# Performance work log

Hardware: AMD Instinct MI355X
Metric: run time of the kernel (lower is better)

Reference implementation:

```python
import jax, jax.numpy as jnp
import numpy as np

N_NODES = 50000


def _gcn_conv(x, edge_index, W, b, n_nodes):
    # PyG GCNConv: add self loops, symmetric normalization, then
    # out[dst] = sum_{src->dst} norm * (x[src] @ W) + b
    src, dst = edge_index[0], edge_index[1]
    loop = jnp.arange(n_nodes, dtype=src.dtype)
    src = jnp.concatenate([src, loop])
    dst = jnp.concatenate([dst, loop])
    deg = jax.ops.segment_sum(jnp.ones_like(src, dtype=x.dtype), dst, num_segments=n_nodes)
    dinv = jnp.where(deg > 0, jax.lax.rsqrt(deg), 0.0)
    norm = dinv[src] * dinv[dst]                      # [E+N]
    h = x @ W                                         # [N, out] dense GEMM first (in >= out here)
    msg = h[src] * norm[:, None]                      # gather + scale
    out = jax.ops.segment_sum(msg, dst, num_segments=n_nodes)  # scatter-add
    return out + b


def setup_inputs() -> dict:
    key = jax.random.key(0)
    k = jax.random.split(key, 5)
    in_c, hid_c, out_c = 128, 128, 64
    n, e = N_NODES, 800000
    x = jax.random.normal(k[0], (n, in_c), dtype=jnp.float32)
    edge_index = jax.random.randint(k[1], (2, e), 0, n, dtype=jnp.int64)
    # Glorot-ish scaled weights
    W1 = jax.random.normal(k[2], (in_c, hid_c), dtype=jnp.float32) * (1.0 / np.sqrt(in_c))
    b1 = jnp.zeros((hid_c,), dtype=jnp.float32)
    W2 = jax.random.normal(k[3], (hid_c, out_c), dtype=jnp.float32) * (1.0 / np.sqrt(hid_c))
    b2 = jnp.zeros((out_c,), dtype=jnp.float32)
    return {"x": x, "edge_index": edge_index, "W1": W1, "b1": b1, "W2": W2, "b2": b2}


def reference(x, edge_index, W1, b1, W2, b2):
    # Net.encode: conv1 -> relu -> conv2
    h = _gcn_conv(x, edge_index, W1, b1, N_NODES)
    h = jax.nn.relu(h)
    z = _gcn_conv(h, edge_index, W2, b2, N_NODES)
    return z
```

## Files before the change

### kernel.cpp

```cpp
#include <hip/hip_runtime.h>
#include <math.h>

constexpr int C_IN  = 128;
constexpr int C_HID = 128;
constexpr int C_OUT = 64;
constexpr int NREP  = 8;

typedef short bf8   __attribute__((ext_vector_type(8)));
typedef float f32x4 __attribute__((ext_vector_type(4)));

__device__ __forceinline__ int wave_incl_scan(int v, int lane) {
    #pragma unroll
    for (int off = 1; off < 64; off <<= 1) {
        int u = __shfl_up(v, off, 64);
        if (lane >= off) v += u;
    }
    return v;
}
__device__ __forceinline__ short b16(float f) {
    unsigned int u = __float_as_uint(f);
    u += 0x7FFFu + ((u >> 16) & 1u);
    return (short)(u >> 16);
}
__device__ __forceinline__ unsigned int bpack(float a, float b) {
    unsigned int ua = __float_as_uint(a), ub = __float_as_uint(b);
    ua += 0x7FFFu + ((ua >> 16) & 1u);
    ub += 0x7FFFu + ((ub >> 16) & 1u);
    return (ua >> 16) | (ub & 0xFFFF0000u);
}
__device__ __forceinline__ void acc4(float* a, const uint2 v) {
    a[0] += __uint_as_float(v.x << 16);
    a[1] += __uint_as_float(v.x & 0xFFFF0000u);
    a[2] += __uint_as_float(v.y << 16);
    a[3] += __uint_as_float(v.y & 0xFFFF0000u);
}
__device__ __forceinline__ void acc8(float* a, const uint4 v) {
    a[0] += __uint_as_float(v.x << 16);
    a[1] += __uint_as_float(v.x & 0xFFFF0000u);
    a[2] += __uint_as_float(v.y << 16);
    a[3] += __uint_as_float(v.y & 0xFFFF0000u);
    a[4] += __uint_as_float(v.z << 16);
    a[5] += __uint_as_float(v.z & 0xFFFF0000u);
    a[6] += __uint_as_float(v.w << 16);
    a[7] += __uint_as_float(v.w & 0xFFFF0000u);
}

__global__ __launch_bounds__(256) void k_zero(int* __restrict__ p, int n4) {
    int i = blockIdx.x * 256 + threadIdx.x;
    if (i < n4) reinterpret_cast<int4*>(p)[i] = make_int4(0, 0, 0, 0);
}

__global__ __launch_bounds__(256) void k_count2r(const int* __restrict__ dst, int e, int n,
                                                 int* __restrict__ cntr,
                                                 int* __restrict__ slot) {
    int i = blockIdx.x * 256 + threadIdx.x;
    if (i >= e) return;
    int r = blockIdx.x & (NREP - 1);
    slot[i] = atomicAdd(&cntr[r * n + dst[i]], 1);
}

__global__ __launch_bounds__(256) void k_scanA8(int* __restrict__ cntr, int n,
                                                int* __restrict__ rowstart,
                                                int* __restrict__ blocksum,
                                                float* __restrict__ dinv) {
    __shared__ int swave[4];
    const int tid = threadIdx.x, lane = tid & 63, w = tid >> 6;
    const int idx = blockIdx.x * 1024 + tid * 4;
    int4 c = make_int4(0, 0, 0, 0);
    if (idx + 3 < n) {
        #pragma unroll
        for (int r = 0; r < NREP; ++r) {
            int4* p = reinterpret_cast<int4*>(cntr + (size_t)r * n + idx);
            int4 t = *p;
            *p = c;
            c.x += t.x; c.y += t.y; c.z += t.z; c.w += t.w;
        }
    } else if (idx < n) {
        for (int m = idx; m < n; ++m) {
            int acc = 0;
            #pragma unroll
            for (int r = 0; r < NREP; ++r) {
                int t = cntr[(size_t)r * n + m];
                cntr[(size_t)r * n + m] = acc;
                acc += t;
            }
            int q = m - idx;
            if (q == 0) c.x = acc; else if (q == 1) c.y = acc;
            else if (q == 2) c.z = acc; else c.w = acc;
        }
    }
    if (idx + 0 < n) dinv[idx + 0] = rsqrtf((float)(c.x + 1));
    if (idx + 1 < n) dinv[idx + 1] = rsqrtf((float)(c.y + 1));
    if (idx + 2 < n) dinv[idx + 2] = rsqrtf((float)(c.z + 1));
    if (idx + 3 < n) dinv[idx + 3] = rsqrtf((float)(c.w + 1));

    const int s4 = c.x + c.y + c.z + c.w;
    const int incl = wave_incl_scan(s4, lane);
    if (lane == 63) swave[w] = incl;
    __syncthreads();
    int base = incl - s4;
    #pragma unroll
    for (int j = 0; j < 4; ++j) if (j < w) base += swave[j];

    int4 o;
    o.x = base;
    o.y = base + c.x;
    o.z = base + c.x + c.y;
    o.w = base + c.x + c.y + c.z;
    if (idx < n) *reinterpret_cast<int4*>(rowstart + idx) = o;

    if (tid == 0) blocksum[blockIdx.x] = swave[0] + swave[1] + swave[2] + swave[3];
}

__global__ __launch_bounds__(64) void k_scanB(const int* __restrict__ blocksum, int nb,
                                              int* __restrict__ blockoff,
                                              int* __restrict__ rowstart, int n) {
    const int lane = threadIdx.x;
    int v = (lane < nb) ? blocksum[lane] : 0;
    int incl = wave_incl_scan(v, lane);
    if (lane < nb) blockoff[lane] = incl - v;
    if (lane == 63) rowstart[n] = incl;
}

__global__ __launch_bounds__(256) void k_scanC(int* __restrict__ rowstart,
                                               const int* __restrict__ blockoff, int n) {
    const int idx = (blockIdx.x * 256 + threadIdx.x) * 4;
    if (idx >= n) return;
    const int off = blockoff[idx >> 10];
    if (idx + 3 < n) {
        int4 v = *reinterpret_cast<int4*>(rowstart + idx);
        v.x += off; v.y += off; v.z += off; v.w += off;
        *reinterpret_cast<int4*>(rowstart + idx) = v;
    } else {
        for (int i = idx; i < n; ++i) rowstart[i] += off;
    }
}

__global__ __launch_bounds__(256) void k_fill2r(const int* __restrict__ src,
                                                const int* __restrict__ dst,
                                                const int* __restrict__ slot, int e, int n,
                                                const int* __restrict__ rowstart,
                                                const int* __restrict__ repoff,
                                                unsigned short* __restrict__ nbr) {
    int i = blockIdx.x * 256 + threadIdx.x;
    if (i >= e) return;
    int r = blockIdx.x & (NREP - 1);
    int d = dst[i];
    int pos = rowstart[d] + repoff[r * n + d] + slot[i];
    nbr[pos] = (unsigned short)src[i];
}

__global__ __launch_bounds__(256) void k_gemm1m(const float* __restrict__ x,
                                                const float* __restrict__ W,
                                                const float* __restrict__ dinv,
                                                unsigned short* __restrict__ h1b,
                                                int n) {
    __shared__ short wf[8 * 4 * 64 * 8];
    const int tid = threadIdx.x;

    for (int i = tid; i < 2048; i += 256) {
        const int l = i & 63, kt = (i >> 6) & 3, ct = i >> 8;
        const int krow = kt * 32 + ((l >> 4) << 3);
        const int col  = ct * 16 + (l & 15);
        const float* wp = W + (size_t)krow * C_HID + col;
        uint4 u;
        u.x = bpack(wp[0 * C_HID], wp[1 * C_HID]);
        u.y = bpack(wp[2 * C_HID], wp[3 * C_HID]);
        u.z = bpack(wp[4 * C_HID], wp[5 * C_HID]);
        u.w = bpack(wp[6 * C_HID], wp[7 * C_HID]);
        reinterpret_cast<uint4*>(wf)[i] = u;
    }
    __syncthreads();

    const int l = tid & 63, w = tid >> 6;
    const int row0 = blockIdx.x * 64 + w * 16;
    int arow = row0 + (l & 15);
    if (arow >= n) arow = n - 1;
    const float* xr = x + (size_t)arow * C_IN + ((l >> 4) << 3);

    bf8 a[4];
    #pragma unroll
    for (int kt = 0; kt < 4; ++kt) {
        float4 p0 = *reinterpret_cast<const float4*>(xr + kt * 32);
        float4 p1 = *reinterpret_cast<const float4*>(xr + kt * 32 + 4);
        bf8 t;
        t[0] = b16(p0.x); t[1] = b16(p0.y); t[2] = b16(p0.z); t[3] = b16(p0.w);
        t[4] = b16(p1.x); t[5] = b16(p1.y); t[6] = b16(p1.z); t[7] = b16(p1.w);
        a[kt] = t;
    }

    f32x4 acc[8];
    #pragma unroll
    for (int ct = 0; ct < 8; ++ct) acc[ct] = (f32x4){0.f, 0.f, 0.f, 0.f};
    const bf8* bw = reinterpret_cast<const bf8*>(wf);
    #pragma unroll
    for (int kt = 0; kt < 4; ++kt)
        #pragma unroll
        for (int ct = 0; ct < 8; ++ct)
            acc[ct] = __builtin_amdgcn_mfma_f32_16x16x32_bf16(
                a[kt], bw[(ct * 4 + kt) * 64 + l], acc[ct], 0, 0, 0);

    const int rbase = row0 + ((l >> 4) << 2);
    float dv[4];
    #pragma unroll
    for (int r = 0; r < 4; ++r) {
        int rr = rbase + r;
        dv[r] = (rr < n) ? dinv[rr] : 0.f;
    }
    #pragma unroll
    for (int ct = 0; ct < 8; ++ct) {
        const int col = ct * 16 + (l & 15);
        #pragma unroll
        for (int r = 0; r < 4; ++r) {
            int rr = rbase + r;
            if (rr < n)
                h1b[(size_t)rr * C_HID + col] = (unsigned short)b16(acc[ct][r] * dv[r]);
        }
    }
}

__global__ __launch_bounds__(256) void k_agg1b(const unsigned int* __restrict__ h1b,
                                               const int* __restrict__ rowstart,
                                               const unsigned short* __restrict__ nbr,
                                               const float* __restrict__ dinv,
                                               const float* __restrict__ b1,
                                               unsigned int* __restrict__ actb,
                                               int n) {
    int node = blockIdx.x * 8 + (threadIdx.x >> 5);
    if (node >= n) return;
    const int c4 = threadIdx.x & 31;
    const uint2* h1v = reinterpret_cast<const uint2*>(h1b);
    float a[4] = {0.f, 0.f, 0.f, 0.f};
    acc4(a, h1v[node * 32 + c4]);
    int j   = rowstart[node];
    int end = rowstart[node + 1];
    for (; j + 1 < end; j += 2) {
        int s0 = nbr[j], s1 = nbr[j + 1];
        uint2 v0 = h1v[s0 * 32 + c4];
        uint2 v1 = h1v[s1 * 32 + c4];
        acc4(a, v0); acc4(a, v1);
    }
    if (j < end) acc4(a, h1v[nbr[j] * 32 + c4]);
    const float sc = dinv[node];
    const float4 bb = reinterpret_cast<const float4*>(b1)[c4];
    uint2 p;
    p.x = bpack(fmaxf(sc * a[0] + bb.x, 0.f), fmaxf(sc * a[1] + bb.y, 0.f));
    p.y = bpack(fmaxf(sc * a[2] + bb.z, 0.f), fmaxf(sc * a[3] + bb.w, 0.f));
    reinterpret_cast<uint2*>(actb)[node * 32 + c4] = p;
}

__global__ __launch_bounds__(256) void k_gemm2m(const unsigned short* __restrict__ actb,
                                                const float* __restrict__ W2,
                                                const float* __restrict__ dinv,
                                                unsigned short* __restrict__ h2b,
                                                int n) {
    __shared__ short wf[4 * 4 * 64 * 8];
    const int tid = threadIdx.x;

    for (int i = tid; i < 1024; i += 256) {
        const int l = i & 63, kt = (i >> 6) & 3, ct = i >> 8;
        const int krow = kt * 32 + ((l >> 4) << 3);
        const int col  = ct * 16 + (l & 15);
        const float* wp = W2 + (size_t)krow * C_OUT + col;
        uint4 u;
        u.x = bpack(wp[0 * C_OUT], wp[1 * C_OUT]);
        u.y = bpack(wp[2 * C_OUT], wp[3 * C_OUT]);
        u.z = bpack(wp[4 * C_OUT], wp[5 * C_OUT]);
        u.w = bpack(wp[6 * C_OUT], wp[7 * C_OUT]);
        reinterpret_cast<uint4*>(wf)[i] = u;
    }
    __syncthreads();

    const int l = tid & 63, w = tid >> 6;
    const int row0 = blockIdx.x * 64 + w * 16;
    int arow = row0 + (l & 15);
    if (arow >= n) arow = n - 1;
    const unsigned short* ar = actb + (size_t)arow * C_HID + ((l >> 4) << 3);

    bf8 a[4];
    #pragma unroll
    for (int kt = 0; kt < 4; ++kt)
        a[kt] = *reinterpret_cast<const bf8*>(ar + kt * 32);

    f32x4 acc[4];
    #pragma unroll
    for (int ct = 0; ct < 4; ++ct) acc[ct] = (f32x4){0.f, 0.f, 0.f, 0.f};
    const bf8* bw = reinterpret_cast<const bf8*>(wf);
    #pragma unroll
    for (int kt = 0; kt < 4; ++kt)
        #pragma unroll
        for (int ct = 0; ct < 4; ++ct)
            acc[ct] = __builtin_amdgcn_mfma_f32_16x16x32_bf16(
                a[kt], bw[(ct * 4 + kt) * 64 + l], acc[ct], 0, 0, 0);

    const int rbase = row0 + ((l >> 4) << 2);
    float dv[4];
    #pragma unroll
    for (int r = 0; r < 4; ++r) {
        int rr = rbase + r;
        dv[r] = (rr < n) ? dinv[rr] : 0.f;
    }
    #pragma unroll
    for (int ct = 0; ct < 4; ++ct) {
        const int col = ct * 16 + (l & 15);
        #pragma unroll
        for (int r = 0; r < 4; ++r) {
            int rr = rbase + r;
            if (rr < n)
                h2b[(size_t)rr * C_OUT + col] = (unsigned short)b16(acc[ct][r] * dv[r]);
        }
    }
}

__global__ __launch_bounds__(256) void k_agg2b(const unsigned int* __restrict__ h2b,
                                               const int* __restrict__ rowstart,
                                               const unsigned short* __restrict__ nbr,
                                               const float* __restrict__ dinv,
                                               const float* __restrict__ b2,
                                               float* __restrict__ outb, int n) {
    int node = blockIdx.x * 32 + (threadIdx.x >> 3);
    if (node >= n) return;
    const int lane8 = threadIdx.x & 7;
    const uint4* h2v = reinterpret_cast<const uint4*>(h2b);
    float a8[8] = {0.f, 0.f, 0.f, 0.f, 0.f, 0.f, 0.f, 0.f};
    acc8(a8, h2v[node * 8 + lane8]);
    int j   = rowstart[node];
    int end = rowstart[node + 1];
    for (; j + 1 < end; j += 2) {
        int s0 = nbr[j], s1 = nbr[j + 1];
        uint4 v0 = h2v[s0 * 8 + lane8];
        uint4 v1 = h2v[s1 * 8 + lane8];
        acc8(a8, v0); acc8(a8, v1);
    }
    if (j < end) acc8(a8, h2v[nbr[j] * 8 + lane8]);
    const float s = dinv[node];
    const float4 c0 = reinterpret_cast<const float4*>(b2)[2 * lane8 + 0];
    const float4 c1 = reinterpret_cast<const float4*>(b2)[2 * lane8 + 1];
    float4 o0, o1;
    o0.x = s * a8[0] + c0.x; o0.y = s * a8[1] + c0.y;
    o0.z = s * a8[2] + c0.z; o0.w = s * a8[3] + c0.w;
    o1.x = s * a8[4] + c1.x; o1.y = s * a8[5] + c1.y;
    o1.z = s * a8[6] + c1.z; o1.w = s * a8[7] + c1.w;
    reinterpret_cast<float4*>(outb)[node * 16 + 2 * lane8 + 0] = o0;
    reinterpret_cast<float4*>(outb)[node * 16 + 2 * lane8 + 1] = o1;
}

extern "C" void kernel_launch(void* const* d_in, const int* in_sizes, int n_in,
                              void* d_out, int out_size, void* d_ws, size_t ws_size,
                              hipStream_t stream) {
    const float* x  = (const float*)d_in[0];
    const int*   ei = (const int*)d_in[1];
    const float* W1 = (const float*)d_in[2];
    const float* b1 = (const float*)d_in[3];
    const float* W2 = (const float*)d_in[4];
    const float* b2 = (const float*)d_in[5];

    const int n = in_sizes[0] / C_IN;
    const int e = in_sizes[1] / 2;
    const int* src = ei;
    const int* dst = ei + e;

    char* ws = (char*)d_ws;
    float* dinv     = (float*)(ws);
    int*   rowstart = (int*)  (ws + (2u << 18));
    int*   blocksum = (int*)  (ws + (1u << 20));
    int*   blockoff = (int*)  (ws + (1u << 20) + 4096);
    int*   cntr     = (int*)  (ws + (2u << 20));
    int*   slot     = (int*)  (ws + (4u << 20));
    unsigned short* nbr  = (unsigned short*)(ws + (8u << 20));
    unsigned short* h1b  = (unsigned short*)(ws + (10u << 20));
    unsigned short* actb = (unsigned short*)(ws + (23u << 20));
    unsigned short* h2b  = (unsigned short*)(ws + (36u << 20));
    float* outb     = (float*)d_out;

    const int NB = (n + 1023) / 1024;
    const int nz4 = (NREP * n + 3) / 4;

    k_zero   <<<(nz4 + 255) / 256, 256, 0, stream>>>(cntr, nz4);
    k_count2r<<<(e + 255) / 256, 256, 0, stream>>>(dst, e, n, cntr, slot);
    k_scanA8 <<<NB, 256, 0, stream>>>(cntr, n, rowstart, blocksum, dinv);
    k_scanB  <<<1, 64, 0, stream>>>(blocksum, NB, blockoff, rowstart, n);
    k_scanC  <<<NB, 256, 0, stream>>>(rowstart, blockoff, n);
    k_fill2r <<<(e + 255) / 256, 256, 0, stream>>>(src, dst, slot, e, n, rowstart, cntr, nbr);
    k_gemm1m <<<(n + 63) / 64, 256, 0, stream>>>(x, W1, dinv, h1b, n);
    k_agg1b  <<<(n + 7) / 8,   256, 0, stream>>>((const unsigned int*)h1b, rowstart, nbr, dinv, b1,
                                                 (unsigned int*)actb, n);
    k_gemm2m <<<(n + 63) / 64, 256, 0, stream>>>(actb, W2, dinv, h2b, n);
    k_agg2b  <<<(n + 31) / 32, 256, 0, stream>>>((const unsigned int*)h2b, rowstart, nbr, dinv, b2,
                                                 outb, n);
}
```

Baseline: 139.7 us.

## Merge scan kernels via last-block ticket, vectorize CSR build and widen agg1 loads

The three scan kernels become one, and the cross-block offset scan is done by the last block to finish, found with an atomic ticket. Consumers now add blockoff on the fly instead of running a separate fix-up pass. The edge count and fill kernels each handle four edges per thread with int4 loads. The layer-1 aggregation uses 16 lanes with 16-byte loads per node instead of 32 lanes with 8-byte loads. This removes two launches and the extra rowstart pass, at the cost of extra blockoff lookups in the gather and aggregation kernels and reliance on threadfence ordering.

```diff
diff --git a/kernel.cpp b/kernel.cpp
--- a/kernel.cpp
+++ b/kernel.cpp
@@ -27,12 +27,6 @@
     ua += 0x7FFFu + ((ua >> 16) & 1u);
     ub += 0x7FFFu + ((ub >> 16) & 1u);
     return (ua >> 16) | (ub & 0xFFFF0000u);
-}
-__device__ __forceinline__ void acc4(float* a, const uint2 v) {
-    a[0] += __uint_as_float(v.x << 16);
-    a[1] += __uint_as_float(v.x & 0xFFFF0000u);
-    a[2] += __uint_as_float(v.y << 16);
-    a[3] += __uint_as_float(v.y & 0xFFFF0000u);
 }
 __device__ __forceinline__ void acc8(float* a, const uint4 v) {
     a[0] += __uint_as_float(v.x << 16);
@@ -50,20 +44,35 @@
     if (i < n4) reinterpret_cast<int4*>(p)[i] = make_int4(0, 0, 0, 0);
 }
 
-__global__ __launch_bounds__(256) void k_count2r(const int* __restrict__ dst, int e, int n,
-                                                 int* __restrict__ cntr,
-                                                 int* __restrict__ slot) {
+__global__ __launch_bounds__(256) void k_count2r4(const int* __restrict__ dst, int e, int n,
+                                                  int* __restrict__ cntr,
+                                                  int* __restrict__ slot) {
     int i = blockIdx.x * 256 + threadIdx.x;
-    if (i >= e) return;
+    int base = i * 4;
+    if (base >= e) return;
     int r = blockIdx.x & (NREP - 1);
-    slot[i] = atomicAdd(&cntr[r * n + dst[i]], 1);
-}
-
-__global__ __launch_bounds__(256) void k_scanA8(int* __restrict__ cntr, int n,
-                                                int* __restrict__ rowstart,
-                                                int* __restrict__ blocksum,
-                                                float* __restrict__ dinv) {
+    int* c = cntr + (size_t)r * n;
+    if (base + 3 < e) {
+        int4 d4 = *reinterpret_cast<const int4*>(dst + base);
+        int4 s4;
+        s4.x = atomicAdd(&c[d4.x], 1);
+        s4.y = atomicAdd(&c[d4.y], 1);
+        s4.z = atomicAdd(&c[d4.z], 1);
+        s4.w = atomicAdd(&c[d4.w], 1);
+        *reinterpret_cast<int4*>(slot + base) = s4;
+    } else {
+        for (int q = base; q < e; ++q) slot[q] = atomicAdd(&c[dst[q]], 1);
+    }
+}
+
+__global__ __launch_bounds__(256) void k_scanAB8(int* __restrict__ cntr, int n,
+                                                 int* __restrict__ rowstart,
+                                                 int* __restrict__ blocksum,
+                                                 int* __restrict__ blockoff,
+                                                 int* __restrict__ ticket,
+                                                 float* __restrict__ dinv) {
     __shared__ int swave[4];
+    __shared__ int amLast;
     const int tid = threadIdx.x, lane = tid & 63, w = tid >> 6;
     const int idx = blockIdx.x * 1024 + tid * 4;
     int4 c = make_int4(0, 0, 0, 0);
@@ -102,52 +111,64 @@
     #pragma unroll
     for (int j = 0; j < 4; ++j) if (j < w) base += swave[j];
 
-    int4 o;
-    o.x = base;
-    o.y = base + c.x;
-    o.z = base + c.x + c.y;
-    o.w = base + c.x + c.y + c.z;
-    if (idx < n) *reinterpret_cast<int4*>(rowstart + idx) = o;
-
-    if (tid == 0) blocksum[blockIdx.x] = swave[0] + swave[1] + swave[2] + swave[3];
-}
-
-__global__ __launch_bounds__(64) void k_scanB(const int* __restrict__ blocksum, int nb,
-                                              int* __restrict__ blockoff,
-                                              int* __restrict__ rowstart, int n) {
-    const int lane = threadIdx.x;
-    int v = (lane < nb) ? blocksum[lane] : 0;
-    int incl = wave_incl_scan(v, lane);
-    if (lane < nb) blockoff[lane] = incl - v;
-    if (lane == 63) rowstart[n] = incl;
-}
-
-__global__ __launch_bounds__(256) void k_scanC(int* __restrict__ rowstart,
-                                               const int* __restrict__ blockoff, int n) {
-    const int idx = (blockIdx.x * 256 + threadIdx.x) * 4;
-    if (idx >= n) return;
-    const int off = blockoff[idx >> 10];
     if (idx + 3 < n) {
-        int4 v = *reinterpret_cast<int4*>(rowstart + idx);
-        v.x += off; v.y += off; v.z += off; v.w += off;
-        *reinterpret_cast<int4*>(rowstart + idx) = v;
+        int4 o;
+        o.x = base;
+        o.y = base + c.x;
+        o.z = base + c.x + c.y;
+        o.w = base + c.x + c.y + c.z;
+        *reinterpret_cast<int4*>(rowstart + idx) = o;
+    } else if (idx < n) {
+        int acc = base;
+        if (idx + 0 < n) { rowstart[idx + 0] = acc; acc += c.x; }
+        if (idx + 1 < n) { rowstart[idx + 1] = acc; acc += c.y; }
+        if (idx + 2 < n) { rowstart[idx + 2] = acc; acc += c.z; }
+        if (idx + 3 < n) { rowstart[idx + 3] = acc; }
+    }
+
+    if (tid == 0) {
+        int tot = swave[0] + swave[1] + swave[2] + swave[3];
+        blocksum[blockIdx.x] = tot;
+        if (blockIdx.x == gridDim.x - 1) rowstart[n] = tot;
+        __threadfence();
+        amLast = (atomicAdd(ticket, 1) == (int)gridDim.x - 1);
+    }
+    __syncthreads();
+    if (amLast && tid < 64) {
+        volatile int* bs = blocksum;
+        const int nb = gridDim.x;
+        int v = (tid < nb) ? bs[tid] : 0;
+        int incl2 = wave_incl_scan(v, tid);
+        if (tid < nb) blockoff[tid] = incl2 - v;
+    }
+}
+
+__global__ __launch_bounds__(256) void k_fill2r4(const int* __restrict__ src,
+                                                 const int* __restrict__ dst,
+                                                 const int* __restrict__ slot, int e, int n,
+                                                 const int* __restrict__ rowstart,
+                                                 const int* __restrict__ blockoff,
+                                                 const int* __restrict__ repoff,
+                                                 unsigned short* __restrict__ nbr) {
+    int i = blockIdx.x * 256 + threadIdx.x;
+    int base = i * 4;
+    if (base >= e) return;
+    int r = blockIdx.x & (NREP - 1);
+    const int* rep = repoff + (size_t)r * n;
+    if (base + 3 < e) {
+        int4 d4 = *reinterpret_cast<const int4*>(dst + base);
+        int4 s4 = *reinterpret_cast<const int4*>(src + base);
+        int4 t4 = *reinterpret_cast<const int4*>(slot + base);
+        nbr[rowstart[d4.x] + blockoff[d4.x >> 10] + rep[d4.x] + t4.x] = (unsigned short)s4.x;
+        nbr[rowstart[d4.y] + blockoff[d4.y >> 10] + rep[d4.y] + t4.y] = (unsigned short)s4.y;
+        nbr[rowstart[d4.z] + blockoff[d4.z >> 10] + rep[d4.z] + t4.z] = (unsigned short)s4.z;
+        nbr[rowstart[d4.w] + blockoff[d4.w >> 10] + rep[d4.w] + t4.w] = (unsigned short)s4.w;
     } else {
-        for (int i = idx; i < n; ++i) rowstart[i] += off;
-    }
-}
-
-__global__ __launch_bounds__(256) void k_fill2r(const int* __restrict__ src,
-                                                const int* __restrict__ dst,
-                                                const int* __restrict__ slot, int e, int n,
-                                                const int* __restrict__ rowstart,
-                                                const int* __restrict__ repoff,
-                                                unsigned short* __restrict__ nbr) {
-    int i = blockIdx.x * 256 + threadIdx.x;
-    if (i >= e) return;
-    int r = blockIdx.x & (NREP - 1);
-    int d = dst[i];
-    int pos = rowstart[d] + repoff[r * n + d] + slot[i];
-    nbr[pos] = (unsigned short)src[i];
+        for (int q = base; q < e; ++q) {
+            int d = dst[q];
+            nbr[rowstart[d] + blockoff[d >> 10] + rep[d] + slot[q]] = (unsigned short)src[q];
+        }
+    }
 }
 
 __global__ __launch_bounds__(256) void k_gemm1m(const float* __restrict__ x,
@@ -219,34 +240,37 @@
     }
 }
 
-__global__ __launch_bounds__(256) void k_agg1b(const unsigned int* __restrict__ h1b,
-                                               const int* __restrict__ rowstart,
-                                               const unsigned short* __restrict__ nbr,
-                                               const float* __restrict__ dinv,
-                                               const float* __restrict__ b1,
-                                               unsigned int* __restrict__ actb,
-                                               int n) {
-    int node = blockIdx.x * 8 + (threadIdx.x >> 5);
+__global__ __launch_bounds__(256) void k_agg1b16(const uint4* __restrict__ h1v,
+                                                 const int* __restrict__ rowstart,
+                                                 const int* __restrict__ blockoff,
+                                                 const unsigned short* __restrict__ nbr,
+                                                 const float* __restrict__ dinv,
+                                                 const float* __restrict__ b1,
+                                                 uint4* __restrict__ actb,
+                                                 int n) {
+    int node = blockIdx.x * 16 + (threadIdx.x >> 4);
     if (node >= n) return;
-    const int c4 = threadIdx.x & 31;
-    const uint2* h1v = reinterpret_cast<const uint2*>(h1b);
-    float a[4] = {0.f, 0.f, 0.f, 0.f};
-    acc4(a, h1v[node * 32 + c4]);
-    int j   = rowstart[node];
-    int end = rowstart[node + 1];
+    const int c8 = threadIdx.x & 15;
+    float a8[8] = {0.f, 0.f, 0.f, 0.f, 0.f, 0.f, 0.f, 0.f};
+    acc8(a8, h1v[(size_t)node * 16 + c8]);
+    int j   = rowstart[node]     + blockoff[node >> 10];
+    int end = rowstart[node + 1] + blockoff[(node + 1) >> 10];
     for (; j + 1 < end; j += 2) {
         int s0 = nbr[j], s1 = nbr[j + 1];
-        uint2 v0 = h1v[s0 * 32 + c4];
-        uint2 v1 = h1v[s1 * 32 + c4];
-        acc4(a, v0); acc4(a, v1);
-    }
-    if (j < end) acc4(a, h1v[nbr[j] * 32 + c4]);
+        uint4 v0 = h1v[(size_t)s0 * 16 + c8];
+        uint4 v1 = h1v[(size_t)s1 * 16 + c8];
+        acc8(a8, v0); acc8(a8, v1);
+    }
+    if (j < end) acc8(a8, h1v[(size_t)nbr[j] * 16 + c8]);
     const float sc = dinv[node];
-    const float4 bb = reinterpret_cast<const float4*>(b1)[c4];
-    uint2 p;
-    p.x = bpack(fmaxf(sc * a[0] + bb.x, 0.f), fmaxf(sc * a[1] + bb.y, 0.f));
-    p.y = bpack(fmaxf(sc * a[2] + bb.z, 0.f), fmaxf(sc * a[3] + bb.w, 0.f));
-    reinterpret_cast<uint2*>(actb)[node * 32 + c4] = p;
+    const float4 bb0 = reinterpret_cast<const float4*>(b1)[2 * c8 + 0];
+    const float4 bb1 = reinterpret_cast<const float4*>(b1)[2 * c8 + 1];
+    uint4 p;
+    p.x = bpack(fmaxf(sc * a8[0] + bb0.x, 0.f), fmaxf(sc * a8[1] + bb0.y, 0.f));
+    p.y = bpack(fmaxf(sc * a8[2] + bb0.z, 0.f), fmaxf(sc * a8[3] + bb0.w, 0.f));
+    p.z = bpack(fmaxf(sc * a8[4] + bb1.x, 0.f), fmaxf(sc * a8[5] + bb1.y, 0.f));
+    p.w = bpack(fmaxf(sc * a8[6] + bb1.z, 0.f), fmaxf(sc * a8[7] + bb1.w, 0.f));
+    actb[(size_t)node * 16 + c8] = p;
 }
 
 __global__ __launch_bounds__(256) void k_gemm2m(const unsigned short* __restrict__ actb,
@@ -312,8 +336,9 @@
     }
 }
 
-__global__ __launch_bounds__(256) void k_agg2b(const unsigned int* __restrict__ h2b,
+__global__ __launch_bounds__(256) void k_agg2b(const uint4* __restrict__ h2v,
                                                const int* __restrict__ rowstart,
+                                               const int* __restrict__ blockoff,
                                                const unsigned short* __restrict__ nbr,
                                                const float* __restrict__ dinv,
                                                const float* __restrict__ b2,
@@ -321,18 +346,17 @@
     int node = blockIdx.x * 32 + (threadIdx.x >> 3);
     if (node >= n) return;
     const int lane8 = threadIdx.x & 7;
-    const uint4* h2v = reinterpret_cast<const uint4*>(h2b);
     float a8[8] = {0.f, 0.f, 0.f, 0.f, 0.f, 0.f, 0.f, 0.f};
-    acc8(a8, h2v[node * 8 + lane8]);
-    int j   = rowstart[node];
-    int end = rowstart[node + 1];
+    acc8(a8, h2v[(size_t)node * 8 + lane8]);
+    int j   = rowstart[node]     + blockoff[node >> 10];
+    int end = rowstart[node + 1] + blockoff[(node + 1) >> 10];
     for (; j + 1 < end; j += 2) {
         int s0 = nbr[j], s1 = nbr[j + 1];
-        uint4 v0 = h2v[s0 * 8 + lane8];
-        uint4 v1 = h2v[s1 * 8 + lane8];
+        uint4 v0 = h2v[(size_t)s0 * 8 + lane8];
+        uint4 v1 = h2v[(size_t)s1 * 8 + lane8];
         acc8(a8, v0); acc8(a8, v1);
     }
-    if (j < end) acc8(a8, h2v[nbr[j] * 8 + lane8]);
+    if (j < end) acc8(a8, h2v[(size_t)nbr[j] * 8 + lane8]);
     const float s = dinv[node];
     const float4 c0 = reinterpret_cast<const float4*>(b2)[2 * lane8 + 0];
     const float4 c1 = reinterpret_cast<const float4*>(b2)[2 * lane8 + 1];
@@ -371,21 +395,22 @@
     unsigned short* h1b  = (unsigned short*)(ws + (10u << 20));
     unsigned short* actb = (unsigned short*)(ws + (23u << 20));
     unsigned short* h2b  = (unsigned short*)(ws + (36u << 20));
+    int*   ticket   = cntr + (size_t)NREP * n;
     float* outb     = (float*)d_out;
 
-    const int NB = (n + 1023) / 1024;
-    const int nz4 = (NREP * n + 3) / 4;
-
-    k_zero   <<<(nz4 + 255) / 256, 256, 0, stream>>>(cntr, nz4);
-    k_count2r<<<(e + 255) / 256, 256, 0, stream>>>(dst, e, n, cntr, slot);
-    k_scanA8 <<<NB, 256, 0, stream>>>(cntr, n, rowstart, blocksum, dinv);
-    k_scanB  <<<1, 64, 0, stream>>>(blocksum, NB, blockoff, rowstart, n);
-    k_scanC  <<<NB, 256, 0, stream>>>(rowstart, blockoff, n);
-    k_fill2r <<<(e + 255) / 256, 256, 0, stream>>>(src, dst, slot, e, n, rowstart, cntr, nbr);
-    k_gemm1m <<<(n + 63) / 64, 256, 0, stream>>>(x, W1, dinv, h1b, n);
-    k_agg1b  <<<(n + 7) / 8,   256, 0, stream>>>((const unsigned int*)h1b, rowstart, nbr, dinv, b1,
-                                                 (unsigned int*)actb, n);
-    k_gemm2m <<<(n + 63) / 64, 256, 0, stream>>>(actb, W2, dinv, h2b, n);
-    k_agg2b  <<<(n + 31) / 32, 256, 0, stream>>>((const unsigned int*)h2b, rowstart, nbr, dinv, b2,
-                                                 outb, n);
-}
+    const int NB  = (n + 1023) / 1024;
+    const int nz4 = (NREP * n + 4 + 3) / 4;
+    const int nE4 = (e + 3) / 4;
+
+    k_zero    <<<(nz4 + 255) / 256, 256, 0, stream>>>(cntr, nz4);
+    k_count2r4<<<(nE4 + 255) / 256, 256, 0, stream>>>(dst, e, n, cntr, slot);
+    k_scanAB8 <<<NB, 256, 0, stream>>>(cntr, n, rowstart, blocksum, blockoff, ticket, dinv);
+    k_fill2r4 <<<(nE4 + 255) / 256, 256, 0, stream>>>(src, dst, slot, e, n, rowstart,
+                                                      blockoff, cntr, nbr);
+    k_gemm1m  <<<(n + 63) / 64, 256, 0, stream>>>(x, W1, dinv, h1b, n);
+    k_agg1b16 <<<(n + 15) / 16, 256, 0, stream>>>((const uint4*)h1b, rowstart, blockoff, nbr,
+                                                  dinv, b1, (uint4*)actb, n);
+    k_gemm2m  <<<(n + 63) / 64, 256, 0, stream>>>(actb, W2, dinv, h2b, n);
+    k_agg2b   <<<(n + 31) / 32, 256, 0, stream>>>((const uint4*)h2b, rowstart, blockoff, nbr,
+                                                  dinv, b2, outb, n);
+}
```

Result: faster. 133.9 us (-4.1%).
